# Optimization experiments

Hardware: AMD Instinct MI355X
Metric: run time of the kernel (lower is better)

Reference implementation:

```python
import jax, jax.numpy as jnp
import numpy as np

N = 20000        # nodes
E = 160000       # directed edges (before self loops)
NODE_DIM = 1287
HEADS = 4
C1, C2, C3 = 128, 256, 128
ACT_SLOPE = 0.15   # module's LeakyReLU between layers
GAT_SLOPE = 0.2    # PyG GATConv default negative_slope


def _gat_layer(x, src, dst, W, att_src, att_dst, bias, heads, out_dim, concat):
    # x: [N, in] ; W: [in, heads*out] ; att_*: [heads, out] ; bias: [heads*out] or [out]
    h = (x @ W).reshape(N, heads, out_dim)                      # [N, H, C]
    a_s = jnp.einsum('nhc,hc->nh', h, att_src)                  # [N, H]
    a_d = jnp.einsum('nhc,hc->nh', h, att_dst)                  # [N, H]
    e = jax.nn.leaky_relu(a_s[src] + a_d[dst], GAT_SLOPE)       # [Etot, H]
    # segment softmax over incoming edges of each dst node (self loops => no empty segments)
    m = jax.ops.segment_max(e, dst, num_segments=N)             # [N, H]
    w = jnp.exp(e - m[dst])
    den = jax.ops.segment_sum(w, dst, num_segments=N)           # [N, H]
    alpha = w / den[dst]                                        # [Etot, H]
    msg = h[src] * alpha[:, :, None]                            # [Etot, H, C]
    out = jax.ops.segment_sum(msg, dst, num_segments=N)         # [N, H, C]
    out = out.reshape(N, heads * out_dim) if concat else out.mean(axis=1)
    return out + bias


def setup_inputs() -> dict:
    key = jax.random.key(0)
    ks = jax.random.split(key, 22)
    s = 0.05
    x = jax.random.normal(ks[0], (N, NODE_DIM), jnp.float32)
    edge_index = jax.random.randint(ks[1], (2, E), 0, N, dtype=jnp.int64)
    inp = {
        'x': x, 'edge_index': edge_index,
        'W1': jax.random.normal(ks[2], (NODE_DIM, HEADS * C1), jnp.float32) * s,
        'as1': jax.random.normal(ks[3], (HEADS, C1), jnp.float32) * s,
        'ad1': jax.random.normal(ks[4], (HEADS, C1), jnp.float32) * s,
        'b1': jnp.zeros((HEADS * C1,), jnp.float32),
        'W2': jax.random.normal(ks[5], (HEADS * C1, HEADS * C2), jnp.float32) * s,
        'as2': jax.random.normal(ks[6], (HEADS, C2), jnp.float32) * s,
        'ad2': jax.random.normal(ks[7], (HEADS, C2), jnp.float32) * s,
        'b2': jnp.zeros((HEADS * C2,), jnp.float32),
        # conv3: 1024 -> 128, 1 head, no concat
        'W3': jax.random.normal(ks[8], (HEADS * C2, C3), jnp.float32) * s,
        'as3': jax.random.normal(ks[9], (1, C3), jnp.float32) * s,
        'ad3': jax.random.normal(ks[10], (1, C3), jnp.float32) * s,
        'b3': jnp.zeros((C3,), jnp.float32),
        # pre_fc: 128 -> 16
        'pw': jax.random.normal(ks[11], (C3, 16), jnp.float32) * s,
        'pb': jnp.zeros((16,), jnp.float32),
        # fc fallback: Linear(16,32) -> LeakyReLU(0.15) -> Linear(32,2)
        'f1w': jax.random.normal(ks[12], (16, 32), jnp.float32) * s,
        'f1b': jnp.zeros((32,), jnp.float32),
        'f2w': jax.random.normal(ks[13], (32, 2), jnp.float32) * s,
        'f2b': jnp.zeros((2,), jnp.float32),
    }
    return inp


def reference(x, edge_index, W1, as1, ad1, b1, W2, as2, ad2, b2,
              W3, as3, ad3, b3, pw, pb, f1w, f1b, f2w, f2b):
    loop = jnp.arange(N, dtype=edge_index.dtype)
    src = jnp.concatenate([edge_index[0], loop])   # PyG add_self_loops=True
    dst = jnp.concatenate([edge_index[1], loop])
    h = _gat_layer(x, src, dst, W1, as1, ad1, b1, HEADS, C1, True)
    h = jax.nn.leaky_relu(h, ACT_SLOPE)            # dropout = identity (eval)
    h = _gat_layer(h, src, dst, W2, as2, ad2, b2, HEADS, C2, True)
    h = jax.nn.leaky_relu(h, ACT_SLOPE)
    h = _gat_layer(h, src, dst, W3, as3, ad3, b3, 1, C3, False)
    h = jax.nn.leaky_relu(h, ACT_SLOPE)
    h = h @ pw + pb                                 # pre_fc (128 -> 16)
    h = jax.nn.leaky_relu(h @ f1w + f1b, ACT_SLOPE)
    return h @ f2w + f2b                            # [N, 2] logits
```

## Files before the change

### kernel.cpp

```cpp
#include <hip/hip_runtime.h>
#include <hip/hip_bf16.h>
#include <cstdint>
#include <cstddef>

#define LRELU(x, s) ((x) > 0.f ? (x) : (s) * (x))

typedef __attribute__((ext_vector_type(8))) short bf16x8;
typedef __attribute__((ext_vector_type(4))) float f32x4;

__device__ __forceinline__ float bflo(uint v) { return __uint_as_float(v << 16); }
__device__ __forceinline__ float bfhi(uint v) { return __uint_as_float(v & 0xffff0000u); }
__device__ __forceinline__ ushort f2bf(float f) {
  const uint u = __float_as_uint(f);
  return (ushort)((u + 0x7fffu + ((u >> 16) & 1u)) >> 16);
}
__device__ __forceinline__ float rl_f(float x, int j) {
  return __uint_as_float(__builtin_amdgcn_readlane(__float_as_uint(x), j));
}

__device__ __forceinline__ void async16(const ushort* g, ushort* l) {
  __builtin_amdgcn_global_load_lds(
      (const __attribute__((address_space(1))) unsigned int*)g,
      (__attribute__((address_space(3))) unsigned int*)l, 16, 0, 0);
}

#define WAITCNT_VM(n) (0xF70 | (n))

__global__ __launch_bounds__(256) void prep_all(
    const float* __restrict__ x, ushort* __restrict__ xb,
    const float* __restrict__ W1, ushort* __restrict__ W1t,
    const float* __restrict__ W2, ushort* __restrict__ W2t,
    const float* __restrict__ W3, ushort* __restrict__ W3t,
    int* __restrict__ deg,
    int N, int K1, int K1p, int nA, int nB, int nC, int nD) {
  __shared__ float tile[32][33];
  const int tid = threadIdx.x;
  int b = blockIdx.x;
  if (b < nA) {
    const int P4 = K1p >> 2;
    const long long idx = (long long)b * 256 + tid;
    if (idx < (long long)N * P4) {
      const int r = (int)(idx / P4);
      const int c = ((int)(idx - (long long)r * P4)) << 2;
      const float* p = x + (size_t)r * K1 + c;
      float v0 = 0.f, v1 = 0.f, v2 = 0.f, v3 = 0.f;
      if (c + 3 < K1) { v0 = p[0]; v1 = p[1]; v2 = p[2]; v3 = p[3]; }
      else {
        if (c + 0 < K1) v0 = p[0];
        if (c + 1 < K1) v1 = p[1];
        if (c + 2 < K1) v2 = p[2];
        if (c + 3 < K1) v3 = p[3];
      }
      uint2 o;
      o.x = (uint)f2bf(v0) | ((uint)f2bf(v1) << 16);
      o.y = (uint)f2bf(v2) | ((uint)f2bf(v3) << 16);
      *(uint2*)(xb + (size_t)r * K1p + c) = o;
    }
    return;
  }
  b -= nA;
  const float* W; ushort* Wt; int K, Nn, Kp, tilesK;
  if (b < nB)           { W = W1; Wt = W1t; K = K1;   Nn = 512;  Kp = K1p;  tilesK = K1p / 32; }
  else if (b < nB + nC) { b -= nB; W = W2; Wt = W2t; K = 512;  Nn = 1024; Kp = 512;  tilesK = 16; }
  else if (b < nB + nC + nD) { b -= nB + nC; W = W3; Wt = W3t; K = 1024; Nn = 128; Kp = 1024; tilesK = 32; }
  else {
    const int i = (b - nB - nC - nD) * 256 + tid;
    if (i < N) deg[i] = 0;
    return;
  }
  const int kt = (b % tilesK) * 32;
  const int nt = (b / tilesK) * 32;
  const int tx = tid & 31, ty = tid >> 5;
  for (int r = ty; r < 32; r += 8) {
    const int k = kt + r, nn = nt + tx;
    tile[r][tx] = (k < K && nn < Nn) ? W[(size_t)k * Nn + nn] : 0.f;
  }
  __syncthreads();
  for (int r = ty; r < 32; r += 8) {
    const int nn = nt + r, k = kt + tx;
    if (nn < Nn && k < Kp) Wt[(size_t)nn * Kp + k] = f2bf(tile[tx][r]);
  }
}

template <int TM, int TAG>
__global__ __launch_bounds__(256) void gemm_bf16(
    const ushort* __restrict__ A, const ushort* __restrict__ Bt, ushort* __restrict__ C,
    int M, int N, int Kp) {
  constexpr int MI = TM / 32;
  constexpr int LPG = (TM == 128) ? 4 : 3;
  __shared__ ushort sA[3 * TM * 32];
  __shared__ ushort sB[3 * 128 * 32];
  const int tid = threadIdx.x;
  const int wave = tid >> 6;
  const int lane = tid & 63;
  const int tilesN = N >> 7;
  const int nwg = gridDim.x;
  const int q8 = nwg >> 3, r8 = nwg & 7;
  const int xcd = blockIdx.x & 7;
  const int lid = blockIdx.x >> 3;
  const int wg = (xcd < r8 ? xcd * (q8 + 1) : r8 * (q8 + 1) + (xcd - r8) * q8) + lid;
  const int bx = wg % tilesN;
  const int by = wg / tilesN;
  const int wrow = (wave >> 1) * (TM / 2);
  const int wcol = (wave & 1) * 64;
  const int quad = lane >> 4;
  const int ml = lane & 15;

  const int seg = (((lane & 3) ^ ((lane >> 3) & 3)) * 8);
  const int rB0 = wave * 32 + (lane >> 2);
  const int gB0 = bx * 128 + rB0;
  const ushort* pB0 = Bt + (size_t)gB0 * Kp + seg;
  const ushort* pB1 = Bt + (size_t)(gB0 + 16) * Kp + seg;
  ushort* lB0 = &sB[(wave * 32) * 32];
  ushort* lB1 = &sB[(wave * 32 + 16) * 32];
  const ushort *pA0, *pA1;
  ushort *lA0, *lA1;
  if constexpr (TM == 128) {
    const int r0 = wave * 32 + (lane >> 2);
    pA0 = A + (size_t)min(by * TM + r0, M - 1) * Kp + seg;
    pA1 = A + (size_t)min(by * TM + r0 + 16, M - 1) * Kp + seg;
    lA0 = &sA[(wave * 32) * 32];
    lA1 = &sA[(wave * 32 + 16) * 32];
  } else {
    const int r0 = wave * 16 + (lane >> 2);
    pA0 = A + (size_t)min(by * TM + r0, M - 1) * Kp + seg;
    pA1 = nullptr;
    lA0 = &sA[(wave * 16) * 32];
    lA1 = nullptr;
  }

  const int nIter = Kp >> 5;
  auto issue = [&](int it, int p) {
    const int k0 = it << 5;
    const int oa = p * TM * 32;
    const int ob_ = p * 128 * 32;
    async16(pA0 + k0, lA0 + oa);
    if constexpr (TM == 128) async16(pA1 + k0, lA1 + oa);
    async16(pB0 + k0, lB0 + ob_);
    async16(pB1 + k0, lB1 + ob_);
  };

  f32x4 acc[MI][4];
#pragma unroll
  for (int mi = 0; mi < MI; mi++)
#pragma unroll
    for (int ni = 0; ni < 4; ni++)
#pragma unroll
      for (int e = 0; e < 4; e++) acc[mi][ni][e] = 0.f;

  const int rq = (quad ^ ((ml >> 1) & 3)) * 8;

  issue(0, 0);
  if (nIter > 1) issue(1, 1);
  int b = 0;
  for (int it = 0; it < nIter; ++it) {
    if (it + 1 < nIter) __builtin_amdgcn_s_waitcnt(WAITCNT_VM(LPG));
    else __builtin_amdgcn_s_waitcnt(WAITCNT_VM(0));
    __builtin_amdgcn_s_barrier();
    if (it + 2 < nIter) {
      const int b2 = (b + 2 >= 3) ? b - 1 : b + 2;
      issue(it + 2, b2);
    }
    const ushort* bA = &sA[b * TM * 32];
    const ushort* bB = &sB[b * 128 * 32];
    bf16x8 af[MI], bfr[4];
#pragma unroll
    for (int mi = 0; mi < MI; mi++)
      af[mi] = *(const bf16x8*)&bA[(wrow + mi * 16 + ml) * 32 + rq];
#pragma unroll
    for (int ni = 0; ni < 4; ni++)
      bfr[ni] = *(const bf16x8*)&bB[(wcol + ni * 16 + ml) * 32 + rq];
#pragma unroll
    for (int mi = 0; mi < MI; mi++)
#pragma unroll
      for (int ni = 0; ni < 4; ni++)
        acc[mi][ni] = __builtin_amdgcn_mfma_f32_16x16x32_bf16(af[mi], bfr[ni], acc[mi][ni], 0, 0, 0);
    b = (b + 1 == 3) ? 0 : b + 1;
  }

#pragma unroll
  for (int mi = 0; mi < MI; mi++) {
#pragma unroll
    for (int r = 0; r < 4; r++) {
      const int row = by * TM + wrow + mi * 16 + quad * 4 + r;
      if (row < M) {
#pragma unroll
        for (int ni = 0; ni < 4; ni++) {
          const int col = bx * 128 + wcol + ni * 16 + ml;
          C[(size_t)row * N + col] = f2bf(acc[mi][ni][r]);
        }
      }
    }
  }
}

template <int H, int C>
__global__ __launch_bounds__(256) void att_dots(
    const ushort* __restrict__ hb, const float* __restrict__ AS,
    const float* __restrict__ AD, float* __restrict__ asb, float* __restrict__ adb,
    int Nn) {
  constexpr int HC = H * C;
  constexpr int EPL = HC / 64;
  constexpr int S = C / EPL;
  const int n = blockIdx.x * 4 + (threadIdx.x >> 6);
  const int lane = threadIdx.x & 63;
  if (n >= Nn) return;
  const int head = lane / S;
  const int cbase = (lane % S) * EPL;
  const ushort* row = hb + (size_t)n * HC + lane * EPL;
  const float* as_h = AS + head * C;
  const float* ad_h = AD + head * C;
  float ps = 0.f, pd = 0.f;
#pragma unroll
  for (int j = 0; j < EPL; j += 2) {
    const uint v = *(const uint*)(row + j);
    const float lo = bflo(v), hi = bfhi(v);
    ps += lo * as_h[cbase + j] + hi * as_h[cbase + j + 1];
    pd += lo * ad_h[cbase + j] + hi * ad_h[cbase + j + 1];
  }
#pragma unroll
  for (int off = 1; off < S; off <<= 1) {
    ps += __shfl_xor(ps, off);
    pd += __shfl_xor(pd, off);
  }
  if ((lane % S) == 0) {
    asb[n * H + head] = ps;
    adb[n * H + head] = pd;
  }
}

__global__ void count_deg(const int* __restrict__ dst, int E, int* __restrict__ deg) {
  const int t = blockIdx.x * blockDim.x + threadIdx.x;
  if (t < E) atomicAdd(&deg[dst[t]], 1);
}

__global__ __launch_bounds__(1024) void scan_kernel(const int* __restrict__ deg,
                                                    int* __restrict__ rowptr,
                                                    int* __restrict__ cursor, int n) {
  __shared__ int swsum[16];
  __shared__ int carry_s;
  const int t = threadIdx.x;
  const int wv = t >> 6, lane = t & 63;
  if (t == 0) carry_s = 0;
  __syncthreads();
  for (int base = 0; base < n; base += 1024) {
    const int i = base + t;
    const int v = (i < n) ? (deg[i] + 1) : 0;
    int sc = v;
#pragma unroll
    for (int off = 1; off < 64; off <<= 1) {
      const int u = __shfl_up(sc, off);
      if (lane >= off) sc += u;
    }
    if (lane == 63) swsum[wv] = sc;
    __syncthreads();
    if (t < 16) {
      int x = swsum[t];
#pragma unroll
      for (int off = 1; off < 16; off <<= 1) {
        const int u = __shfl_up(x, off);
        if (t >= off) x += u;
      }
      swsum[t] = x;
    }
    __syncthreads();
    const int incl = sc + (wv == 0 ? 0 : swsum[wv - 1]) + carry_s;
    if (i < n) { rowptr[i + 1] = incl; cursor[i] = incl - v; }
    if (base == 0 && t == 0) rowptr[0] = 0;
    __syncthreads();
    if (t == 0) carry_s += swsum[15];
    __syncthreads();
  }
}

__global__ void scatter_edges(const int* __restrict__ esrc, const int* __restrict__ edst,
                              int E, int Etot, int* __restrict__ cursor,
                              int* __restrict__ csr_src) {
  const int t = blockIdx.x * blockDim.x + threadIdx.x;
  if (t >= Etot) return;
  int s, d;
  if (t < E) { s = esrc[t]; d = edst[t]; } else { s = t - E; d = s; }
  const int pos = atomicAdd(&cursor[d], 1);
  csr_src[pos] = s;
}

template <int H, int C>
__global__ __launch_bounds__(256) void gat_agg_wave(
    const ushort* __restrict__ hb, const int* __restrict__ rowptr,
    const int* __restrict__ csr_src, const float* __restrict__ a_s,
    const float* __restrict__ a_d, const float* __restrict__ bias,
    ushort* __restrict__ outb, float act_slope, int Nn) {
  constexpr int HC = H * C;
  constexpr int NU = HC / 2;
  constexpr int UPT = NU / 256;
  constexpr int GRP = (UPT == 2) ? 4 : 8;
  const int n = blockIdx.x * 4 + (threadIdx.x >> 6);
  const int lane = threadIdx.x & 63;
  if (n >= Nn) return;
  float ad_n[H];
#pragma unroll
  for (int h = 0; h < H; h++) ad_n[h] = a_d[n * H + h];
  const int start = rowptr[n], end = rowptr[n + 1];
  f32x4 acc[UPT][2];
#pragma unroll
  for (int q = 0; q < UPT; q++)
#pragma unroll
    for (int u = 0; u < 2; u++)
#pragma unroll
      for (int e = 0; e < 4; e++) acc[q][u][e] = 0.f;
  float den[H];
#pragma unroll
  for (int h = 0; h < H; h++) den[h] = 0.f;

  for (int base = start; base < end; base += 64) {
    const int cnt = min(64, end - base);
    int s = 0;
// ... 66 lines not shown
        acc[q][1][0] += wq * bflo(v.z);
        acc[q][1][1] += wq * bfhi(v.z);
        acc[q][1][2] += wq * bflo(v.w);
        acc[q][1][3] += wq * bfhi(v.w);
      }
    }
  }
#pragma unroll
  for (int h = 0; h < H; h++) {
#pragma unroll
    for (int off = 1; off < 64; off <<= 1) den[h] += __shfl_xor(den[h], off);
    den[h] = 1.f / den[h];
  }
#pragma unroll
  for (int q = 0; q < UPT; q++) {
    const int e0 = q * 512 + 8 * lane;
    const float iv = den[e0 / C];
    const float4 ba = *(const float4*)(bias + e0);
    const float4 bb = *(const float4*)(bias + e0 + 4);
    const float o0 = LRELU(acc[q][0][0] * iv + ba.x, act_slope);
    const float o1 = LRELU(acc[q][0][1] * iv + ba.y, act_slope);
    const float o2 = LRELU(acc[q][0][2] * iv + ba.z, act_slope);
    const float o3 = LRELU(acc[q][0][3] * iv + ba.w, act_slope);
    const float o4 = LRELU(acc[q][1][0] * iv + bb.x, act_slope);
    const float o5 = LRELU(acc[q][1][1] * iv + bb.y, act_slope);
    const float o6 = LRELU(acc[q][1][2] * iv + bb.z, act_slope);
    const float o7 = LRELU(acc[q][1][3] * iv + bb.w, act_slope);
    uint4 o;
    o.x = (uint)f2bf(o0) | ((uint)f2bf(o1) << 16);
    o.y = (uint)f2bf(o2) | ((uint)f2bf(o3) << 16);
    o.z = (uint)f2bf(o4) | ((uint)f2bf(o5) << 16);
    o.w = (uint)f2bf(o6) | ((uint)f2bf(o7) << 16);
    ((uint4*)outb)[(size_t)n * (NU / 4) + q * 64 + lane] = o;
  }
}

__global__ __launch_bounds__(256) void gat_agg3_mlp(
    const ushort* __restrict__ hb, const int* __restrict__ rowptr,
    const int* __restrict__ csr_src, const float* __restrict__ a_s,
    const float* __restrict__ a_d, const float* __restrict__ b3,
    const float* __restrict__ pw, const float* __restrict__ pb,
    const float* __restrict__ f1w, const float* __restrict__ f1b,
    const float* __restrict__ f2w, const float* __restrict__ f2b,
    float* __restrict__ out, int Nn) {
  __shared__ float sx[4][128];
  __shared__ float s1[4][16];
  __shared__ float s2[4][32];
  const int w = threadIdx.x >> 6;
  const int lane = threadIdx.x & 63;
  const int n = blockIdx.x * 4 + w;
  if (n >= Nn) return;
  const float ad_n = a_d[n];
  const int start = rowptr[n], end = rowptr[n + 1];
  float2 acc = make_float2(0.f, 0.f);
  float den = 0.f;
  for (int base = start; base < end; base += 64) {
    const int cnt = min(64, end - base);
    int s = 0;
    float wv_ = 0.f;
    if (lane < cnt) {
      s = csr_src[base + lane];
      float lg = a_s[s] + ad_n;
      lg = LRELU(lg, 0.2f);
      wv_ = __expf(lg);
      den += wv_;
    }
// ... 68 lines not shown
  const float* W2  = (const float*)d_in[6];
  const float* as2 = (const float*)d_in[7];
  const float* ad2 = (const float*)d_in[8];
  const float* b2  = (const float*)d_in[9];
  const float* W3  = (const float*)d_in[10];
  const float* as3 = (const float*)d_in[11];
  const float* ad3 = (const float*)d_in[12];
  const float* b3  = (const float*)d_in[13];
  const float* pw  = (const float*)d_in[14];
  const float* pb  = (const float*)d_in[15];
  const float* f1w = (const float*)d_in[16];
  const float* f1b = (const float*)d_in[17];
  const float* f2w = (const float*)d_in[18];
  const float* f2b = (const float*)d_in[19];
  float* out = (float*)d_out;

  const int N = in_sizes[0] / 1287;
  const int E = in_sizes[1] / 2;
  const int Etot = E + N;
  const int* esrc = ei;
  const int* edst = ei + E;
  const int K1 = 1287, K1p = 1312;

  char* ws = (char*)d_ws;
  size_t off = 0;
  auto alloc = [&](size_t bytes) -> void* {
    void* p = ws + off;
    off = (off + bytes + 255) & ~(size_t)255;
    return p;
  };
  ushort* hb  = (ushort*)alloc((size_t)N * 1024 * 2);
  ushort* ob  = (ushort*)alloc((size_t)N * 1024 * 2);
  ushort* xb  = (ushort*)alloc((size_t)N * K1p * 2);
  ushort* W1t = (ushort*)alloc((size_t)512 * K1p * 2);
  ushort* W2t = (ushort*)alloc((size_t)1024 * 512 * 2);
  ushort* W3t = (ushort*)alloc((size_t)128 * 1024 * 2);
  float* av   = (float*)alloc((size_t)N * 8 * sizeof(float));
  int* deg    = (int*)alloc((size_t)N * sizeof(int));
  int* rowptr = (int*)alloc((size_t)(N + 1) * sizeof(int));
  int* cursor = (int*)alloc((size_t)N * sizeof(int));
  int* csr    = (int*)alloc((size_t)Etot * sizeof(int));
  float* asb = av;
  float* adb = av + (size_t)N * 4;

  const int nA = (int)(((long long)N * (K1p / 4) + 255) / 256);
  const int nB = (K1p / 32) * (512 / 32);
  const int nC = (512 / 32) * (1024 / 32);
  const int nD = (1024 / 32) * (128 / 32);
  const int nE = (N + 255) / 256;
  prep_all<<<nA + nB + nC + nD + nE, 256, 0, stream>>>(
      x, xb, W1, W1t, W2, W2t, W3, W3t, deg, N, K1, K1p, nA, nB, nC, nD);

  count_deg<<<(E + 255) / 256, 256, 0, stream>>>(edst, E, deg);
  scan_kernel<<<1, 1024, 0, stream>>>(deg, rowptr, cursor, N);
  scatter_edges<<<(Etot + 255) / 256, 256, 0, stream>>>(esrc, edst, E, Etot, cursor, csr);

  const int tilesM = (N + 127) / 128;
  const int tilesM64 = (N + 63) / 64;
  const int nodeBlocks = (N + 3) / 4;

  {
    const int HC = 512;
    gemm_bf16<128, 1><<<tilesM * (HC / 128), 256, 0, stream>>>(xb, W1t, hb, N, HC, K1p);
    att_dots<4, 128><<<nodeBlocks, 256, 0, stream>>>(hb, as1, ad1, asb, adb, N);
    gat_agg_wave<4, 128><<<nodeBlocks, 256, 0, stream>>>(hb, rowptr, csr, asb, adb,
                                                         b1, ob, 0.15f, N);
  }
  {
    const int HC = 1024;
    gemm_bf16<128, 2><<<tilesM * (HC / 128), 256, 0, stream>>>(ob, W2t, hb, N, HC, 512);
    att_dots<4, 256><<<nodeBlocks, 256, 0, stream>>>(hb, as2, ad2, asb, adb, N);
    gat_agg_wave<4, 256><<<nodeBlocks, 256, 0, stream>>>(hb, rowptr, csr, asb, adb,
                                                         b2, ob, 0.15f, N);
  }
  {
    const int HC = 128;
    gemm_bf16<64, 3><<<tilesM64 * (HC / 128), 256, 0, stream>>>(ob, W3t, hb, N, HC, 1024);
    att_dots<1, 128><<<nodeBlocks, 256, 0, stream>>>(hb, as3, ad3, asb, adb, N);
    gat_agg3_mlp<<<nodeBlocks, 256, 0, stream>>>(hb, rowptr, csr, asb, adb, b3,
                                                 pw, pb, f1w, f1b, f2w, f2b, out, N);
  }
}
```

Baseline: 455.4 us.

## Precompute W·att vectors and fuse attention dots and edge scatter into GEMM launches

Attention logits are now computed as x·(W·att) instead of (x·W)·att. The folded W·att vectors are precomputed in the prep kernel, and the per-node dots run as extra blocks inside each GEMM launch, so they no longer wait for the GEMM output. Degree counting moves into the prep kernel, the edge scatter moves into the first GEMM launch, and deg is zeroed with a memset, which removes several small launches and serialization points. In exchange the dot blocks read the wider layer input (1287 and 1024 columns in layers 1 and 3) instead of the narrower GEMM output. Rounding also changes slightly, since the logits no longer come from the bf16-rounded h.

```diff
diff --git a/kernel.cpp b/kernel.cpp
--- a/kernel.cpp
+++ b/kernel.cpp
@@ -31,8 +31,12 @@
     const float* __restrict__ W1, ushort* __restrict__ W1t,
     const float* __restrict__ W2, ushort* __restrict__ W2t,
     const float* __restrict__ W3, ushort* __restrict__ W3t,
-    int* __restrict__ deg,
-    int N, int K1, int K1p, int nA, int nB, int nC, int nD) {
+    const float* __restrict__ as1, const float* __restrict__ ad1,
+    const float* __restrict__ as2, const float* __restrict__ ad2,
+    const float* __restrict__ as3, const float* __restrict__ ad3,
+    float* __restrict__ wasad1, float* __restrict__ wasad2, float* __restrict__ wasad3,
+    const int* __restrict__ edst, int* __restrict__ deg, int E,
+    int N, int K1, int K1p, int nA, int nB, int nC, int nD, int nCnt) {
   __shared__ float tile[32][33];
   const int tid = threadIdx.x;
   int b = blockIdx.x;
@@ -59,33 +63,89 @@
     return;
   }
   b -= nA;
-  const float* W; ushort* Wt; int K, Nn, Kp, tilesK;
-  if (b < nB)           { W = W1; Wt = W1t; K = K1;   Nn = 512;  Kp = K1p;  tilesK = K1p / 32; }
-  else if (b < nB + nC) { b -= nB; W = W2; Wt = W2t; K = 512;  Nn = 1024; Kp = 512;  tilesK = 16; }
-  else if (b < nB + nC + nD) { b -= nB + nC; W = W3; Wt = W3t; K = 1024; Nn = 128; Kp = 1024; tilesK = 32; }
-  else {
-    const int i = (b - nB - nC - nD) * 256 + tid;
-    if (i < N) deg[i] = 0;
+  if (b < nB + nC + nD) {
+    const float* W; ushort* Wt; int K, Nn, Kp, tilesK;
+    if (b < nB)           { W = W1; Wt = W1t; K = K1;   Nn = 512;  Kp = K1p;  tilesK = K1p / 32; }
+    else if (b < nB + nC) { b -= nB; W = W2; Wt = W2t; K = 512;  Nn = 1024; Kp = 512;  tilesK = 16; }
+    else                  { b -= nB + nC; W = W3; Wt = W3t; K = 1024; Nn = 128; Kp = 1024; tilesK = 32; }
+    const int kt = (b % tilesK) * 32;
+    const int nt = (b / tilesK) * 32;
+    const int tx = tid & 31, ty = tid >> 5;
+    for (int r = ty; r < 32; r += 8) {
+      const int k = kt + r, nn = nt + tx;
+      tile[r][tx] = (k < K && nn < Nn) ? W[(size_t)k * Nn + nn] : 0.f;
+    }
+    __syncthreads();
+    for (int r = ty; r < 32; r += 8) {
+      const int nn = nt + r, k = kt + tx;
+      if (nn < Nn && k < Kp) Wt[(size_t)nn * Kp + k] = f2bf(tile[tx][r]);
+    }
     return;
   }
-  const int kt = (b % tilesK) * 32;
-  const int nt = (b / tilesK) * 32;
-  const int tx = tid & 31, ty = tid >> 5;
-  for (int r = ty; r < 32; r += 8) {
-    const int k = kt + r, nn = nt + tx;
-    tile[r][tx] = (k < K && nn < Nn) ? W[(size_t)k * Nn + nn] : 0.f;
-  }
-  __syncthreads();
-  for (int r = ty; r < 32; r += 8) {
-    const int nn = nt + r, k = kt + tx;
-    if (nn < Nn && k < Kp) Wt[(size_t)nn * Kp + k] = f2bf(tile[tx][r]);
-  }
-}
-
-template <int TM, int TAG>
-__global__ __launch_bounds__(256) void gemm_bf16(
+  b -= nB + nC + nD;
+  if (b < nCnt) {
+    const int t = b * 256 + tid;
+    if (t < E) atomicAdd(&deg[edst[t]], 1);
+    return;
+  }
+  b -= nCnt;
+  if (b < 6) {
+    const int k = b * 256 + tid;
+    if (k < K1p) {
+      float s[4] = {0.f, 0.f, 0.f, 0.f}, d[4] = {0.f, 0.f, 0.f, 0.f};
+      if (k < K1) {
+        const float* wrow = W1 + (size_t)k * 512;
+        for (int h = 0; h < 4; h++) {
+          float a = 0.f, c2 = 0.f;
+          for (int c = 0; c < 128; c++) {
+            const float w = wrow[h * 128 + c];
+            a += w * as1[h * 128 + c];
+            c2 += w * ad1[h * 128 + c];
+          }
+          s[h] = a; d[h] = c2;
+        }
+      }
+      for (int h = 0; h < 4; h++) { wasad1[k * 8 + h] = s[h]; wasad1[k * 8 + 4 + h] = d[h]; }
+    }
+    return;
+  }
+  b -= 6;
+  if (b < 2) {
+    const int k = b * 256 + tid;
+    const float* wrow = W2 + (size_t)k * 1024;
+    for (int h = 0; h < 4; h++) {
+      float a = 0.f, c2 = 0.f;
+      for (int c = 0; c < 256; c++) {
+        const float w = wrow[h * 256 + c];
+        a += w * as2[h * 256 + c];
+        c2 += w * ad2[h * 256 + c];
+      }
+      wasad2[k * 8 + h] = a; wasad2[k * 8 + 4 + h] = c2;
+    }
+    return;
+  }
+  b -= 2;
+  {
+    const int k = b * 256 + tid;
+    const float* wrow = W3 + (size_t)k * 128;
+    float a = 0.f, c2 = 0.f;
+    for (int c = 0; c < 128; c++) {
+      const float w = wrow[c];
+      a += w * as3[c];
+      c2 += w * ad3[c];
+    }
+    wasad3[k * 2] = a; wasad3[k * 2 + 1] = c2;
+  }
+}
+
+template <int TM, int H, int TAG>
+__global__ __launch_bounds__(256) void gemm_dots(
     const ushort* __restrict__ A, const ushort* __restrict__ Bt, ushort* __restrict__ C,
-    int M, int N, int Kp) {
+    int M, int N, int Kp, int gemmBlocks,
+    const ushort* __restrict__ dIn, int Kd, const float* __restrict__ wasad,
+    float* __restrict__ asb, float* __restrict__ adb, int dotsBlocks,
+    const int* __restrict__ esrc, const int* __restrict__ edst, int E, int Etot,
+    int* __restrict__ cursor, int* __restrict__ csr_src) {
   constexpr int MI = TM / 32;
   constexpr int LPG = (TM == 128) ? 4 : 3;
   __shared__ ushort sA[3 * TM * 32];
@@ -93,11 +153,59 @@
   const int tid = threadIdx.x;
   const int wave = tid >> 6;
   const int lane = tid & 63;
+  const int blk = blockIdx.x;
+
+  if (blk >= gemmBlocks) {
+    const int db = blk - gemmBlocks;
+    if (db < dotsBlocks) {
+      const int n = db * 4 + wave;
+      if (n >= M) return;
+      float ps[H], pd[H];
+#pragma unroll
+      for (int h = 0; h < H; h++) { ps[h] = 0.f; pd[h] = 0.f; }
+      const uint* xr = (const uint*)(dIn + (size_t)n * Kd);
+      const int NU2 = Kd >> 1;
+      for (int u = lane; u < NU2; u += 64) {
+        const uint v = xr[u];
+        const float lo = bflo(v), hi = bfhi(v);
+        const float* wr = wasad + (size_t)u * (4 * H);
+#pragma unroll
+        for (int h = 0; h < H; h++) {
+          ps[h] += lo * wr[h] + hi * wr[2 * H + h];
+          pd[h] += lo * wr[H + h] + hi * wr[3 * H + h];
+        }
+      }
+#pragma unroll
+      for (int h = 0; h < H; h++) {
+#pragma unroll
+        for (int off = 1; off < 64; off <<= 1) {
+          ps[h] += __shfl_xor(ps[h], off);
+          pd[h] += __shfl_xor(pd[h], off);
+        }
+      }
+      if (lane == 0) {
+#pragma unroll
+        for (int h = 0; h < H; h++) {
+          asb[n * H + h] = ps[h];
+          adb[n * H + h] = pd[h];
+        }
+      }
+    } else {
+      const int t = (db - dotsBlocks) * 256 + tid;
+      if (t >= Etot) return;
+      int s, d;
+      if (t < E) { s = esrc[t]; d = edst[t]; } else { s = t - E; d = s; }
+      const int pos = atomicAdd(&cursor[d], 1);
+      csr_src[pos] = s;
+    }
+    return;
+  }
+
   const int tilesN = N >> 7;
-  const int nwg = gridDim.x;
+  const int nwg = gemmBlocks;
   const int q8 = nwg >> 3, r8 = nwg & 7;
-  const int xcd = blockIdx.x & 7;
-  const int lid = blockIdx.x >> 3;
+  const int xcd = blk & 7;
+  const int lid = blk >> 3;
   const int wg = (xcd < r8 ? xcd * (q8 + 1) : r8 * (q8 + 1) + (xcd - r8) * q8) + lid;
   const int bx = wg % tilesN;
   const int by = wg / tilesN;
@@ -194,46 +302,6 @@
   }
 }
 
-template <int H, int C>
-__global__ __launch_bounds__(256) void att_dots(
-    const ushort* __restrict__ hb, const float* __restrict__ AS,
-    const float* __restrict__ AD, float* __restrict__ asb, float* __restrict__ adb,
-    int Nn) {
-  constexpr int HC = H * C;
-  constexpr int EPL = HC / 64;
-  constexpr int S = C / EPL;
-  const int n = blockIdx.x * 4 + (threadIdx.x >> 6);
-  const int lane = threadIdx.x & 63;
-  if (n >= Nn) return;
-  const int head = lane / S;
-  const int cbase = (lane % S) * EPL;
-  const ushort* row = hb + (size_t)n * HC + lane * EPL;
-  const float* as_h = AS + head * C;
-  const float* ad_h = AD + head * C;
-  float ps = 0.f, pd = 0.f;
-#pragma unroll
-  for (int j = 0; j < EPL; j += 2) {
-    const uint v = *(const uint*)(row + j);
-    const float lo = bflo(v), hi = bfhi(v);
-    ps += lo * as_h[cbase + j] + hi * as_h[cbase + j + 1];
-    pd += lo * ad_h[cbase + j] + hi * ad_h[cbase + j + 1];
-  }
-#pragma unroll
-  for (int off = 1; off < S; off <<= 1) {
-    ps += __shfl_xor(ps, off);
-    pd += __shfl_xor(pd, off);
-  }
-  if ((lane % S) == 0) {
-    asb[n * H + head] = ps;
-    adb[n * H + head] = pd;
-  }
-}
-
-__global__ void count_deg(const int* __restrict__ dst, int E, int* __restrict__ deg) {
-  const int t = blockIdx.x * blockDim.x + threadIdx.x;
-  if (t < E) atomicAdd(&deg[dst[t]], 1);
-}
-
 __global__ __launch_bounds__(1024) void scan_kernel(const int* __restrict__ deg,
                                                     int* __restrict__ rowptr,
                                                     int* __restrict__ cursor, int n) {
@@ -271,17 +339,6 @@
     if (t == 0) carry_s += swsum[15];
     __syncthreads();
   }
-}
-
-__global__ void scatter_edges(const int* __restrict__ esrc, const int* __restrict__ edst,
-                              int E, int Etot, int* __restrict__ cursor,
-                              int* __restrict__ csr_src) {
-  const int t = blockIdx.x * blockDim.x + threadIdx.x;
-  if (t >= Etot) return;
-  int s, d;
-  if (t < E) { s = esrc[t]; d = edst[t]; } else { s = t - E; d = s; }
-  const int pos = atomicAdd(&cursor[d], 1);
-  csr_src[pos] = s;
 }
 
 template <int H, int C>
@@ -556,43 +613,54 @@
   int* rowptr = (int*)alloc((size_t)(N + 1) * sizeof(int));
   int* cursor = (int*)alloc((size_t)N * sizeof(int));
   int* csr    = (int*)alloc((size_t)Etot * sizeof(int));
+  float* wasad1 = (float*)alloc((size_t)K1p * 8 * sizeof(float));
+  float* wasad2 = (float*)alloc((size_t)512 * 8 * sizeof(float));
+  float* wasad3 = (float*)alloc((size_t)1024 * 2 * sizeof(float));
   float* asb = av;
   float* adb = av + (size_t)N * 4;
 
+  hipMemsetAsync(deg, 0, (size_t)N * sizeof(int), stream);
   const int nA = (int)(((long long)N * (K1p / 4) + 255) / 256);
   const int nB = (K1p / 32) * (512 / 32);
   const int nC = (512 / 32) * (1024 / 32);
   const int nD = (1024 / 32) * (128 / 32);
-  const int nE = (N + 255) / 256;
-  prep_all<<<nA + nB + nC + nD + nE, 256, 0, stream>>>(
-      x, xb, W1, W1t, W2, W2t, W3, W3t, deg, N, K1, K1p, nA, nB, nC, nD);
-
-  count_deg<<<(E + 255) / 256, 256, 0, stream>>>(edst, E, deg);
+  const int nCnt = (E + 255) / 256;
+  prep_all<<<nA + nB + nC + nD + nCnt + 6 + 2 + 4, 256, 0, stream>>>(
+      x, xb, W1, W1t, W2, W2t, W3, W3t,
+      as1, ad1, as2, ad2, as3, ad3, wasad1, wasad2, wasad3,
+      edst, deg, E, N, K1, K1p, nA, nB, nC, nD, nCnt);
+
   scan_kernel<<<1, 1024, 0, stream>>>(deg, rowptr, cursor, N);
-  scatter_edges<<<(Etot + 255) / 256, 256, 0, stream>>>(esrc, edst, E, Etot, cursor, csr);
 
   const int tilesM = (N + 127) / 128;
   const int tilesM64 = (N + 63) / 64;
   const int nodeBlocks = (N + 3) / 4;
+  const int scatB = (Etot + 255) / 256;
 
   {
-    const int HC = 512;
-    gemm_bf16<128, 1><<<tilesM * (HC / 128), 256, 0, stream>>>(xb, W1t, hb, N, HC, K1p);
-    att_dots<4, 128><<<nodeBlocks, 256, 0, stream>>>(hb, as1, ad1, asb, adb, N);
+    const int g = tilesM * 4;
+    gemm_dots<128, 4, 1><<<g + nodeBlocks + scatB, 256, 0, stream>>>(
+        xb, W1t, hb, N, 512, K1p, g,
+        xb, K1p, wasad1, asb, adb, nodeBlocks,
+        esrc, edst, E, Etot, cursor, csr);
     gat_agg_wave<4, 128><<<nodeBlocks, 256, 0, stream>>>(hb, rowptr, csr, asb, adb,
                                                          b1, ob, 0.15f, N);
   }
   {
-    const int HC = 1024;
-    gemm_bf16<128, 2><<<tilesM * (HC / 128), 256, 0, stream>>>(ob, W2t, hb, N, HC, 512);
-    att_dots<4, 256><<<nodeBlocks, 256, 0, stream>>>(hb, as2, ad2, asb, adb, N);
+    const int g = tilesM * 8;
+    gemm_dots<128, 4, 2><<<g + nodeBlocks, 256, 0, stream>>>(
+        ob, W2t, hb, N, 1024, 512, g,
+        ob, 512, wasad2, asb, adb, nodeBlocks,
+        nullptr, nullptr, 0, 0, nullptr, nullptr);
     gat_agg_wave<4, 256><<<nodeBlocks, 256, 0, stream>>>(hb, rowptr, csr, asb, adb,
                                                          b2, ob, 0.15f, N);
   }
   {
-    const int HC = 128;
-    gemm_bf16<64, 3><<<tilesM64 * (HC / 128), 256, 0, stream>>>(ob, W3t, hb, N, HC, 1024);
-    att_dots<1, 128><<<nodeBlocks, 256, 0, stream>>>(hb, as3, ad3, asb, adb, N);
+    const int g = tilesM64;
+    gemm_dots<64, 1, 3><<<g + nodeBlocks, 256, 0, stream>>>(
+        ob, W3t, hb, N, 128, 1024, g,
+        ob, 1024, wasad3, asb, adb, nodeBlocks,
+        nullptr, nullptr, 0, 0, nullptr, nullptr);
     gat_agg3_mlp<<<nodeBlocks, 256, 0, stream>>>(hb, rowptr, csr, asb, adb, b3,
                                                  pw, pb, f1w, f1b, f2w, f2b, out, N);
   }
```

New measurement: 523.7 us. 1.15x slower.

## Reorder layer-2 GAT to aggregate before projection and fuse graph-build kernels

Applied to the files above, without the earlier changes.

Layer 2 now aggregates the 512-wide inputs per head first, then multiplies by W2, instead of projecting to 1024 and aggregating that. The attention logits come from precomputed W2·att vectors applied directly to the layer-1 output, and bias plus LeakyReLU move into the GEMM epilogue. This cuts gather traffic in the aggregation (512 vs 1024 bf16 per edge). In exchange it writes a 4x512-per-node intermediate that the GEMM reads with a head-split A offset. Degree counting and edge scatter are folded into the prep kernel and the layer-1 GEMM launch, with a memset replacing the deg-zero blocks, to cut launch count.

```diff
diff --git a/kernel.cpp b/kernel.cpp
--- a/kernel.cpp
+++ b/kernel.cpp
@@ -31,8 +31,10 @@
     const float* __restrict__ W1, ushort* __restrict__ W1t,
     const float* __restrict__ W2, ushort* __restrict__ W2t,
     const float* __restrict__ W3, ushort* __restrict__ W3t,
-    int* __restrict__ deg,
-    int N, int K1, int K1p, int nA, int nB, int nC, int nD) {
+    const float* __restrict__ as2, const float* __restrict__ ad2,
+    float* __restrict__ wasad2,
+    const int* __restrict__ edst, int* __restrict__ deg, int E,
+    int N, int K1, int K1p, int nA, int nB, int nC, int nD, int nCnt) {
   __shared__ float tile[32][33];
   const int tid = threadIdx.x;
   int b = blockIdx.x;
@@ -59,33 +61,54 @@
     return;
   }
   b -= nA;
-  const float* W; ushort* Wt; int K, Nn, Kp, tilesK;
-  if (b < nB)           { W = W1; Wt = W1t; K = K1;   Nn = 512;  Kp = K1p;  tilesK = K1p / 32; }
-  else if (b < nB + nC) { b -= nB; W = W2; Wt = W2t; K = 512;  Nn = 1024; Kp = 512;  tilesK = 16; }
-  else if (b < nB + nC + nD) { b -= nB + nC; W = W3; Wt = W3t; K = 1024; Nn = 128; Kp = 1024; tilesK = 32; }
-  else {
-    const int i = (b - nB - nC - nD) * 256 + tid;
-    if (i < N) deg[i] = 0;
+  if (b < nB + nC + nD) {
+    const float* W; ushort* Wt; int K, Nn, Kp, tilesK;
+    if (b < nB)           { W = W1; Wt = W1t; K = K1;   Nn = 512;  Kp = K1p;  tilesK = K1p / 32; }
+    else if (b < nB + nC) { b -= nB; W = W2; Wt = W2t; K = 512;  Nn = 1024; Kp = 512;  tilesK = 16; }
+    else                  { b -= nB + nC; W = W3; Wt = W3t; K = 1024; Nn = 128; Kp = 1024; tilesK = 32; }
+    const int kt = (b % tilesK) * 32;
+    const int nt = (b / tilesK) * 32;
+    const int tx = tid & 31, ty = tid >> 5;
+    for (int r = ty; r < 32; r += 8) {
+      const int k = kt + r, nn = nt + tx;
+      tile[r][tx] = (k < K && nn < Nn) ? W[(size_t)k * Nn + nn] : 0.f;
+    }
+    __syncthreads();
+    for (int r = ty; r < 32; r += 8) {
+      const int nn = nt + r, k = kt + tx;
+      if (nn < Nn && k < Kp) Wt[(size_t)nn * Kp + k] = f2bf(tile[tx][r]);
+    }
     return;
   }
-  const int kt = (b % tilesK) * 32;
-  const int nt = (b / tilesK) * 32;
-  const int tx = tid & 31, ty = tid >> 5;
-  for (int r = ty; r < 32; r += 8) {
-    const int k = kt + r, nn = nt + tx;
-    tile[r][tx] = (k < K && nn < Nn) ? W[(size_t)k * Nn + nn] : 0.f;
-  }
-  __syncthreads();
-  for (int r = ty; r < 32; r += 8) {
-    const int nn = nt + r, k = kt + tx;
-    if (nn < Nn && k < Kp) Wt[(size_t)nn * Kp + k] = f2bf(tile[tx][r]);
-  }
-}
-
-template <int TM, int TAG>
+  b -= nB + nC + nD;
+  if (b < nCnt) {
+    const int t = b * 256 + tid;
+    if (t < E) atomicAdd(&deg[edst[t]], 1);
+    return;
+  }
+  b -= nCnt;
+  {
+    const int k = b * 256 + tid;
+    const float* wrow = W2 + (size_t)k * 1024;
+    for (int h = 0; h < 4; h++) {
+      float a = 0.f, c2 = 0.f;
+      for (int c = 0; c < 256; c++) {
+        const float w = wrow[h * 256 + c];
+        a += w * as2[h * 256 + c];
+        c2 += w * ad2[h * 256 + c];
+      }
+      wasad2[k * 8 + h] = a; wasad2[k * 8 + 4 + h] = c2;
+    }
+  }
+}
+
+template <int TM, int TAG, bool HSPLIT, bool FUSEACT>
 __global__ __launch_bounds__(256) void gemm_bf16(
     const ushort* __restrict__ A, const ushort* __restrict__ Bt, ushort* __restrict__ C,
-    int M, int N, int Kp) {
+    int M, int N, int Kp, int Astride, const float* __restrict__ bias,
+    int gemmBlocks,
+    const int* __restrict__ esrc, const int* __restrict__ edst, int E, int Etot,
+    int* __restrict__ cursor, int* __restrict__ csr_src) {
   constexpr int MI = TM / 32;
   constexpr int LPG = (TM == 128) ? 4 : 3;
   __shared__ ushort sA[3 * TM * 32];
@@ -93,8 +116,19 @@
   const int tid = threadIdx.x;
   const int wave = tid >> 6;
   const int lane = tid & 63;
+
+  if (blockIdx.x >= gemmBlocks) {
+    const int t = (blockIdx.x - gemmBlocks) * 256 + tid;
+    if (t >= Etot) return;
+    int s, d;
+    if (t < E) { s = esrc[t]; d = edst[t]; } else { s = t - E; d = s; }
+    const int pos = atomicAdd(&cursor[d], 1);
+    csr_src[pos] = s;
+    return;
+  }
+
   const int tilesN = N >> 7;
-  const int nwg = gridDim.x;
+  const int nwg = gemmBlocks;
   const int q8 = nwg >> 3, r8 = nwg & 7;
   const int xcd = blockIdx.x & 7;
   const int lid = blockIdx.x >> 3;
@@ -105,6 +139,7 @@
   const int wcol = (wave & 1) * 64;
   const int quad = lane >> 4;
   const int ml = lane & 15;
+  const int aOff = HSPLIT ? ((bx >> 1) * 512) : 0;
 
   const int seg = (((lane & 3) ^ ((lane >> 3) & 3)) * 8);
   const int rB0 = wave * 32 + (lane >> 2);
@@ -117,13 +152,13 @@
   ushort *lA0, *lA1;
   if constexpr (TM == 128) {
     const int r0 = wave * 32 + (lane >> 2);
-    pA0 = A + (size_t)min(by * TM + r0, M - 1) * Kp + seg;
-    pA1 = A + (size_t)min(by * TM + r0 + 16, M - 1) * Kp + seg;
+    pA0 = A + (size_t)min(by * TM + r0, M - 1) * Astride + aOff + seg;
+    pA1 = A + (size_t)min(by * TM + r0 + 16, M - 1) * Astride + aOff + seg;
     lA0 = &sA[(wave * 32) * 32];
     lA1 = &sA[(wave * 32 + 16) * 32];
   } else {
     const int r0 = wave * 16 + (lane >> 2);
-    pA0 = A + (size_t)min(by * TM + r0, M - 1) * Kp + seg;
+    pA0 = A + (size_t)min(by * TM + r0, M - 1) * Astride + aOff + seg;
     pA1 = nullptr;
     lA0 = &sA[(wave * 16) * 32];
     lA1 = nullptr;
@@ -178,6 +213,11 @@
     b = (b + 1 == 3) ? 0 : b + 1;
   }
 
+  float bv[4];
+  if constexpr (FUSEACT) {
+#pragma unroll
+    for (int ni = 0; ni < 4; ni++) bv[ni] = bias[bx * 128 + wcol + ni * 16 + ml];
+  }
 #pragma unroll
   for (int mi = 0; mi < MI; mi++) {
 #pragma unroll
@@ -187,7 +227,9 @@
 #pragma unroll
         for (int ni = 0; ni < 4; ni++) {
           const int col = bx * 128 + wcol + ni * 16 + ml;
-          C[(size_t)row * N + col] = f2bf(acc[mi][ni][r]);
+          float o = acc[mi][ni][r];
+          if constexpr (FUSEACT) o = LRELU(o + bv[ni], 0.15f);
+          C[(size_t)row * N + col] = f2bf(o);
         }
       }
     }
@@ -229,9 +271,39 @@
   }
 }
 
-__global__ void count_deg(const int* __restrict__ dst, int E, int* __restrict__ deg) {
-  const int t = blockIdx.x * blockDim.x + threadIdx.x;
-  if (t < E) atomicAdd(&deg[dst[t]], 1);
+__global__ __launch_bounds__(256) void att_dots_x(
+    const ushort* __restrict__ dIn, const float* __restrict__ wasad,
+    float* __restrict__ asb, float* __restrict__ adb, int Nn) {
+  const int n = blockIdx.x * 4 + (threadIdx.x >> 6);
+  const int lane = threadIdx.x & 63;
+  if (n >= Nn) return;
+  float ps[4] = {0.f, 0.f, 0.f, 0.f}, pd[4] = {0.f, 0.f, 0.f, 0.f};
+  const uint* xr = (const uint*)(dIn + (size_t)n * 512);
+  for (int u = lane; u < 256; u += 64) {
+    const uint v = xr[u];
+    const float lo = bflo(v), hi = bfhi(v);
+    const float* wr = wasad + (size_t)u * 16;
+#pragma unroll
+    for (int h = 0; h < 4; h++) {
+      ps[h] += lo * wr[h] + hi * wr[8 + h];
+      pd[h] += lo * wr[4 + h] + hi * wr[12 + h];
+    }
+  }
+#pragma unroll
+  for (int h = 0; h < 4; h++) {
+#pragma unroll
+    for (int off = 1; off < 64; off <<= 1) {
+      ps[h] += __shfl_xor(ps[h], off);
+      pd[h] += __shfl_xor(pd[h], off);
+    }
+  }
+  if (lane == 0) {
+#pragma unroll
+    for (int h = 0; h < 4; h++) {
+      asb[n * 4 + h] = ps[h];
+      adb[n * 4 + h] = pd[h];
+    }
+  }
 }
 
 __global__ __launch_bounds__(1024) void scan_kernel(const int* __restrict__ deg,
@@ -271,17 +343,6 @@
     if (t == 0) carry_s += swsum[15];
     __syncthreads();
   }
-}
-
-__global__ void scatter_edges(const int* __restrict__ esrc, const int* __restrict__ edst,
-                              int E, int Etot, int* __restrict__ cursor,
-                              int* __restrict__ csr_src) {
-  const int t = blockIdx.x * blockDim.x + threadIdx.x;
-  if (t >= Etot) return;
-  int s, d;
-  if (t < E) { s = esrc[t]; d = edst[t]; } else { s = t - E; d = s; }
-  const int pos = atomicAdd(&cursor[d], 1);
-  csr_src[pos] = s;
 }
 
 template <int H, int C>
@@ -414,6 +475,110 @@
     o.z = (uint)f2bf(o4) | ((uint)f2bf(o5) << 16);
     o.w = (uint)f2bf(o6) | ((uint)f2bf(o7) << 16);
     ((uint4*)outb)[(size_t)n * (NU / 4) + q * 64 + lane] = o;
+  }
+}
+
+__global__ __launch_bounds__(256) void gat_agg2x(
+    const ushort* __restrict__ ob, const int* __restrict__ rowptr,
+    const int* __restrict__ csr_src, const float* __restrict__ a_s,
+    const float* __restrict__ a_d, ushort* __restrict__ aggx, int Nn) {
+  const int n = blockIdx.x * 4 + (threadIdx.x >> 6);
+  const int lane = threadIdx.x & 63;
+  if (n >= Nn) return;
+  float ad_n[4];
+#pragma unroll
+  for (int h = 0; h < 4; h++) ad_n[h] = a_d[n * 4 + h];
+  const int start = rowptr[n], end = rowptr[n + 1];
+  f32x4 acc[4][2];
+#pragma unroll
+  for (int h = 0; h < 4; h++)
+#pragma unroll
+    for (int u = 0; u < 2; u++)
+#pragma unroll
+      for (int e = 0; e < 4; e++) acc[h][u][e] = 0.f;
+  float den[4] = {0.f, 0.f, 0.f, 0.f};
+
+  for (int base = start; base < end; base += 64) {
+    const int cnt = min(64, end - base);
+    int s = 0;
+    float w[4] = {0.f, 0.f, 0.f, 0.f};
+    if (lane < cnt) {
+      s = csr_src[base + lane];
+      const float4 t4 = *(const float4*)(a_s + s * 4);
+      const float asv[4] = {t4.x, t4.y, t4.z, t4.w};
+#pragma unroll
+      for (int h = 0; h < 4; h++) {
+        float lg = asv[h] + ad_n[h];
+        lg = LRELU(lg, 0.2f);
+        w[h] = __expf(lg);
+        den[h] += w[h];
+      }
+    }
+    const int cntg = cnt & ~3;
+    int j = 0;
+    for (; j < cntg; j += 4) {
+      uint4 v[4];
+#pragma unroll
+      for (int g = 0; g < 4; g++) {
+        const int sj = __builtin_amdgcn_readlane(s, j + g);
+        v[g] = ((const uint4*)(ob + (size_t)sj * 512))[lane];
+      }
+#pragma unroll
+      for (int g = 0; g < 4; g++) {
+        const float l0 = bflo(v[g].x), h0 = bfhi(v[g].x);
+        const float l1 = bflo(v[g].y), h1 = bfhi(v[g].y);
+        const float l2 = bflo(v[g].z), h2 = bfhi(v[g].z);
+        const float l3 = bflo(v[g].w), h3 = bfhi(v[g].w);
+#pragma unroll
+        for (int h = 0; h < 4; h++) {
+          const float wq = rl_f(w[h], j + g);
+          acc[h][0][0] += wq * l0;
+          acc[h][0][1] += wq * h0;
+          acc[h][0][2] += wq * l1;
+          acc[h][0][3] += wq * h1;
+          acc[h][1][0] += wq * l2;
+          acc[h][1][1] += wq * h2;
+          acc[h][1][2] += wq * l3;
+          acc[h][1][3] += wq * h3;
+        }
+      }
+    }
+    for (; j < cnt; j++) {
+      const int sj = __builtin_amdgcn_readlane(s, j);
+      const uint4 v = ((const uint4*)(ob + (size_t)sj * 512))[lane];
+      const float l0 = bflo(v.x), h0 = bfhi(v.x);
+      const float l1 = bflo(v.y), h1 = bfhi(v.y);
+      const float l2 = bflo(v.z), h2 = bfhi(v.z);
+      const float l3 = bflo(v.w), h3 = bfhi(v.w);
+#pragma unroll
+      for (int h = 0; h < 4; h++) {
+        const float wq = rl_f(w[h], j);
+        acc[h][0][0] += wq * l0;
+        acc[h][0][1] += wq * h0;
+        acc[h][0][2] += wq * l1;
+        acc[h][0][3] += wq * h1;
+        acc[h][1][0] += wq * l2;
+        acc[h][1][1] += wq * h2;
+        acc[h][1][2] += wq * l3;
+        acc[h][1][3] += wq * h3;
+      }
+    }
+  }
+#pragma unroll
+  for (int h = 0; h < 4; h++) {
+#pragma unroll
+    for (int off = 1; off < 64; off <<= 1) den[h] += __shfl_xor(den[h], off);
+    den[h] = 1.f / den[h];
+  }
+#pragma unroll
+  for (int h = 0; h < 4; h++) {
+    const float iv = den[h];
+    uint4 o;
+    o.x = (uint)f2bf(acc[h][0][0] * iv) | ((uint)f2bf(acc[h][0][1] * iv) << 16);
+    o.y = (uint)f2bf(acc[h][0][2] * iv) | ((uint)f2bf(acc[h][0][3] * iv) << 16);
+    o.z = (uint)f2bf(acc[h][1][0] * iv) | ((uint)f2bf(acc[h][1][1] * iv) << 16);
+    o.w = (uint)f2bf(acc[h][1][2] * iv) | ((uint)f2bf(acc[h][1][3] * iv) << 16);
+    ((uint4*)(aggx + (size_t)n * 2048 + h * 512))[lane] = o;
   }
 }
 
@@ -548,6 +713,7 @@
   ushort* hb  = (ushort*)alloc((size_t)N * 1024 * 2);
   ushort* ob  = (ushort*)alloc((size_t)N * 1024 * 2);
   ushort* xb  = (ushort*)alloc((size_t)N * K1p * 2);
+  ushort* aggx = (ushort*)alloc((size_t)N * 2048 * 2);
   ushort* W1t = (ushort*)alloc((size_t)512 * K1p * 2);
   ushort* W2t = (ushort*)alloc((size_t)1024 * 512 * 2);
   ushort* W3t = (ushort*)alloc((size_t)128 * 1024 * 2);
@@ -556,42 +722,48 @@
   int* rowptr = (int*)alloc((size_t)(N + 1) * sizeof(int));
   int* cursor = (int*)alloc((size_t)N * sizeof(int));
   int* csr    = (int*)alloc((size_t)Etot * sizeof(int));
+  float* wasad2 = (float*)alloc((size_t)512 * 8 * sizeof(float));
   float* asb = av;
   float* adb = av + (size_t)N * 4;
 
+  hipMemsetAsync(deg, 0, (size_t)N * sizeof(int), stream);
   const int nA = (int)(((long long)N * (K1p / 4) + 255) / 256);
   const int nB = (K1p / 32) * (512 / 32);
   const int nC = (512 / 32) * (1024 / 32);
   const int nD = (1024 / 32) * (128 / 32);
-  const int nE = (N + 255) / 256;
-  prep_all<<<nA + nB + nC + nD + nE, 256, 0, stream>>>(
-      x, xb, W1, W1t, W2, W2t, W3, W3t, deg, N, K1, K1p, nA, nB, nC, nD);
-
-  count_deg<<<(E + 255) / 256, 256, 0, stream>>>(edst, E, deg);
+  const int nCnt = (E + 255) / 256;
+  prep_all<<<nA + nB + nC + nD + nCnt + 2, 256, 0, stream>>>(
+      x, xb, W1, W1t, W2, W2t, W3, W3t, as2, ad2, wasad2,
+      edst, deg, E, N, K1, K1p, nA, nB, nC, nD, nCnt);
+
   scan_kernel<<<1, 1024, 0, stream>>>(deg, rowptr, cursor, N);
-  scatter_edges<<<(Etot + 255) / 256, 256, 0, stream>>>(esrc, edst, E, Etot, cursor, csr);
 
   const int tilesM = (N + 127) / 128;
   const int tilesM64 = (N + 63) / 64;
   const int nodeBlocks = (N + 3) / 4;
+  const int scatB = (Etot + 255) / 256;
 
   {
-    const int HC = 512;
-    gemm_bf16<128, 1><<<tilesM * (HC / 128), 256, 0, stream>>>(xb, W1t, hb, N, HC, K1p);
+    const int g = tilesM * 4;
+    gemm_bf16<128, 1, false, false><<<g + scatB, 256, 0, stream>>>(
+        xb, W1t, hb, N, 512, K1p, K1p, nullptr, g,
+        esrc, edst, E, Etot, cursor, csr);
     att_dots<4, 128><<<nodeBlocks, 256, 0, stream>>>(hb, as1, ad1, asb, adb, N);
     gat_agg_wave<4, 128><<<nodeBlocks, 256, 0, stream>>>(hb, rowptr, csr, asb, adb,
                                                          b1, ob, 0.15f, N);
   }
   {
-    const int HC = 1024;
-    gemm_bf16<128, 2><<<tilesM * (HC / 128), 256, 0, stream>>>(ob, W2t, hb, N, HC, 512);
-    att_dots<4, 256><<<nodeBlocks, 256, 0, stream>>>(hb, as2, ad2, asb, adb, N);
-    gat_agg_wave<4, 256><<<nodeBlocks, 256, 0, stream>>>(hb, rowptr, csr, asb, adb,
-                                                         b2, ob, 0.15f, N);
+    att_dots_x<<<nodeBlocks, 256, 0, stream>>>(ob, wasad2, asb, adb, N);
+    gat_agg2x<<<nodeBlocks, 256, 0, stream>>>(ob, rowptr, csr, asb, adb, aggx, N);
+    const int g = tilesM * 8;
+    gemm_bf16<128, 2, true, true><<<g, 256, 0, stream>>>(
+        aggx, W2t, ob, N, 1024, 512, 2048, b2, g,
+        nullptr, nullptr, 0, 0, nullptr, nullptr);
   }
   {
-    const int HC = 128;
-    gemm_bf16<64, 3><<<tilesM64 * (HC / 128), 256, 0, stream>>>(ob, W3t, hb, N, HC, 1024);
+    gemm_bf16<64, 3, false, false><<<tilesM64, 256, 0, stream>>>(
+        ob, W3t, hb, N, 128, 1024, 1024, nullptr, tilesM64,
+        nullptr, nullptr, 0, 0, nullptr, nullptr);
     att_dots<1, 128><<<nodeBlocks, 256, 0, stream>>>(hb, as3, ad3, asb, adb, N);
     gat_agg3_mlp<<<nodeBlocks, 256, 0, stream>>>(hb, rowptr, csr, asb, adb, b3,
                                                  pw, pb, f1w, f1b, f2w, f2b, out, N);
```

After: 477.7 us. 4.9% more time.

## Fold degree counting into prep kernel and edge scatter into first GEMM

Applied to the files above, without the earlier changes.

Degree counting now runs as extra blocks of the prep kernel, with deg zeroed by a memset beforehand. The CSR edge scatter runs as extra blocks appended to the layer-1 GEMM grid. This removes two separate kernel launches and lets the small atomic-heavy work overlap with the weight prep and the GEMM. The GEMM's XCD workgroup remapping now uses the GEMM block count rather than gridDim, and the extra branch adds kernel arguments and may perturb block scheduling.

```diff
diff --git a/kernel.cpp b/kernel.cpp
--- a/kernel.cpp
+++ b/kernel.cpp
@@ -31,7 +31,7 @@
     const float* __restrict__ W1, ushort* __restrict__ W1t,
     const float* __restrict__ W2, ushort* __restrict__ W2t,
     const float* __restrict__ W3, ushort* __restrict__ W3t,
-    int* __restrict__ deg,
+    const int* __restrict__ edst, int* __restrict__ deg, int E,
     int N, int K1, int K1p, int nA, int nB, int nC, int nD) {
   __shared__ float tile[32][33];
   const int tid = threadIdx.x;
@@ -59,33 +59,38 @@
     return;
   }
   b -= nA;
-  const float* W; ushort* Wt; int K, Nn, Kp, tilesK;
-  if (b < nB)           { W = W1; Wt = W1t; K = K1;   Nn = 512;  Kp = K1p;  tilesK = K1p / 32; }
-  else if (b < nB + nC) { b -= nB; W = W2; Wt = W2t; K = 512;  Nn = 1024; Kp = 512;  tilesK = 16; }
-  else if (b < nB + nC + nD) { b -= nB + nC; W = W3; Wt = W3t; K = 1024; Nn = 128; Kp = 1024; tilesK = 32; }
-  else {
-    const int i = (b - nB - nC - nD) * 256 + tid;
-    if (i < N) deg[i] = 0;
+  if (b < nB + nC + nD) {
+    const float* W; ushort* Wt; int K, Nn, Kp, tilesK;
+    if (b < nB)           { W = W1; Wt = W1t; K = K1;   Nn = 512;  Kp = K1p;  tilesK = K1p / 32; }
+    else if (b < nB + nC) { b -= nB; W = W2; Wt = W2t; K = 512;  Nn = 1024; Kp = 512;  tilesK = 16; }
+    else                  { b -= nB + nC; W = W3; Wt = W3t; K = 1024; Nn = 128; Kp = 1024; tilesK = 32; }
+    const int kt = (b % tilesK) * 32;
+    const int nt = (b / tilesK) * 32;
+    const int tx = tid & 31, ty = tid >> 5;
+    for (int r = ty; r < 32; r += 8) {
+      const int k = kt + r, nn = nt + tx;
+      tile[r][tx] = (k < K && nn < Nn) ? W[(size_t)k * Nn + nn] : 0.f;
+    }
+    __syncthreads();
+    for (int r = ty; r < 32; r += 8) {
+      const int nn = nt + r, k = kt + tx;
+      if (nn < Nn && k < Kp) Wt[(size_t)nn * Kp + k] = f2bf(tile[tx][r]);
+    }
     return;
   }
-  const int kt = (b % tilesK) * 32;
-  const int nt = (b / tilesK) * 32;
-  const int tx = tid & 31, ty = tid >> 5;
-  for (int r = ty; r < 32; r += 8) {
-    const int k = kt + r, nn = nt + tx;
-    tile[r][tx] = (k < K && nn < Nn) ? W[(size_t)k * Nn + nn] : 0.f;
-  }
-  __syncthreads();
-  for (int r = ty; r < 32; r += 8) {
-    const int nn = nt + r, k = kt + tx;
-    if (nn < Nn && k < Kp) Wt[(size_t)nn * Kp + k] = f2bf(tile[tx][r]);
+  b -= nB + nC + nD;
+  {
+    const int t = b * 256 + tid;
+    if (t < E) atomicAdd(&deg[edst[t]], 1);
   }
 }
 
 template <int TM, int TAG>
 __global__ __launch_bounds__(256) void gemm_bf16(
     const ushort* __restrict__ A, const ushort* __restrict__ Bt, ushort* __restrict__ C,
-    int M, int N, int Kp) {
+    int M, int N, int Kp, int gemmBlocks,
+    const int* __restrict__ esrc, const int* __restrict__ edst, int E, int Etot,
+    int* __restrict__ cursor, int* __restrict__ csr_src) {
   constexpr int MI = TM / 32;
   constexpr int LPG = (TM == 128) ? 4 : 3;
   __shared__ ushort sA[3 * TM * 32];
@@ -93,8 +98,19 @@
   const int tid = threadIdx.x;
   const int wave = tid >> 6;
   const int lane = tid & 63;
+
+  if (blockIdx.x >= gemmBlocks) {
+    const int t = (blockIdx.x - gemmBlocks) * 256 + tid;
+    if (t >= Etot) return;
+    int s, d;
+    if (t < E) { s = esrc[t]; d = edst[t]; } else { s = t - E; d = s; }
+    const int pos = atomicAdd(&cursor[d], 1);
+    csr_src[pos] = s;
+    return;
+  }
+
   const int tilesN = N >> 7;
-  const int nwg = gridDim.x;
+  const int nwg = gemmBlocks;
   const int q8 = nwg >> 3, r8 = nwg & 7;
   const int xcd = blockIdx.x & 7;
   const int lid = blockIdx.x >> 3;
@@ -229,11 +245,6 @@
   }
 }
 
-__global__ void count_deg(const int* __restrict__ dst, int E, int* __restrict__ deg) {
-  const int t = blockIdx.x * blockDim.x + threadIdx.x;
-  if (t < E) atomicAdd(&deg[dst[t]], 1);
-}
-
 __global__ __launch_bounds__(1024) void scan_kernel(const int* __restrict__ deg,
                                                     int* __restrict__ rowptr,
                                                     int* __restrict__ cursor, int n) {
@@ -271,17 +282,6 @@
     if (t == 0) carry_s += swsum[15];
     __syncthreads();
   }
-}
-
-__global__ void scatter_edges(const int* __restrict__ esrc, const int* __restrict__ edst,
-                              int E, int Etot, int* __restrict__ cursor,
-                              int* __restrict__ csr_src) {
-  const int t = blockIdx.x * blockDim.x + threadIdx.x;
-  if (t >= Etot) return;
-  int s, d;
-  if (t < E) { s = esrc[t]; d = edst[t]; } else { s = t - E; d = s; }
-  const int pos = atomicAdd(&cursor[d], 1);
-  csr_src[pos] = s;
 }
 
 template <int H, int C>
@@ -559,39 +559,42 @@
   float* asb = av;
   float* adb = av + (size_t)N * 4;
 
+  hipMemsetAsync(deg, 0, (size_t)N * sizeof(int), stream);
   const int nA = (int)(((long long)N * (K1p / 4) + 255) / 256);
   const int nB = (K1p / 32) * (512 / 32);
   const int nC = (512 / 32) * (1024 / 32);
   const int nD = (1024 / 32) * (128 / 32);
-  const int nE = (N + 255) / 256;
-  prep_all<<<nA + nB + nC + nD + nE, 256, 0, stream>>>(
-      x, xb, W1, W1t, W2, W2t, W3, W3t, deg, N, K1, K1p, nA, nB, nC, nD);
-
-  count_deg<<<(E + 255) / 256, 256, 0, stream>>>(edst, E, deg);
+  const int nCnt = (E + 255) / 256;
+  prep_all<<<nA + nB + nC + nD + nCnt, 256, 0, stream>>>(
+      x, xb, W1, W1t, W2, W2t, W3, W3t,
+      edst, deg, E, N, K1, K1p, nA, nB, nC, nD);
+
   scan_kernel<<<1, 1024, 0, stream>>>(deg, rowptr, cursor, N);
-  scatter_edges<<<(Etot + 255) / 256, 256, 0, stream>>>(esrc, edst, E, Etot, cursor, csr);
 
   const int tilesM = (N + 127) / 128;
   const int tilesM64 = (N + 63) / 64;
   const int nodeBlocks = (N + 3) / 4;
+  const int scatB = (Etot + 255) / 256;
 
   {
-    const int HC = 512;
-    gemm_bf16<128, 1><<<tilesM * (HC / 128), 256, 0, stream>>>(xb, W1t, hb, N, HC, K1p);
+    const int g = tilesM * 4;
+    gemm_bf16<128, 1><<<g + scatB, 256, 0, stream>>>(
+        xb, W1t, hb, N, 512, K1p, g, esrc, edst, E, Etot, cursor, csr);
     att_dots<4, 128><<<nodeBlocks, 256, 0, stream>>>(hb, as1, ad1, asb, adb, N);
     gat_agg_wave<4, 128><<<nodeBlocks, 256, 0, stream>>>(hb, rowptr, csr, asb, adb,
                                                          b1, ob, 0.15f, N);
   }
   {
-    const int HC = 1024;
-    gemm_bf16<128, 2><<<tilesM * (HC / 128), 256, 0, stream>>>(ob, W2t, hb, N, HC, 512);
+    const int g = tilesM * 8;
+    gemm_bf16<128, 2><<<g, 256, 0, stream>>>(
+        ob, W2t, hb, N, 1024, 512, g, nullptr, nullptr, 0, 0, nullptr, nullptr);
     att_dots<4, 256><<<nodeBlocks, 256, 0, stream>>>(hb, as2, ad2, asb, adb, N);
     gat_agg_wave<4, 256><<<nodeBlocks, 256, 0, stream>>>(hb, rowptr, csr, asb, adb,
                                                          b2, ob, 0.15f, N);
   }
   {
-    const int HC = 128;
-    gemm_bf16<64, 3><<<tilesM64 * (HC / 128), 256, 0, stream>>>(ob, W3t, hb, N, HC, 1024);
+    gemm_bf16<64, 3><<<tilesM64, 256, 0, stream>>>(
+        ob, W3t, hb, N, 128, 1024, tilesM64, nullptr, nullptr, 0, 0, nullptr, nullptr);
     att_dots<1, 128><<<nodeBlocks, 256, 0, stream>>>(hb, as3, ad3, asb, adb, N);
     gat_agg3_mlp<<<nodeBlocks, 256, 0, stream>>>(hb, rowptr, csr, asb, adb, b3,
                                                  pw, pb, f1w, f1b, f2w, f2b, out, N);
```

Measured after the change: 441.5 us. 1.03x faster.
